# Kernel optimization log

Measured on AMD Instinct MI355X. Metric: run time of the kernel, lower is better.

Reference implementation:

```python
import jax, jax.numpy as jnp
import numpy as np

B, S, D, H = 4, 2048, 256, 8  # batch, seq (context=target), hidden_dim, n_heads


def setup_inputs() -> dict:
    key = jax.random.key(0)
    ks = jax.random.split(key, 12)
    sd = 1.0 / np.sqrt(D)          # torch Linear default init scale (uniform bound)
    sdo = 1.0 / np.sqrt(H * D)
    inp = {
        "k": jax.random.normal(ks[0], (B, S, D), jnp.float32),
        "v": jax.random.normal(ks[1], (B, S, D), jnp.float32),
        "q": jax.random.normal(ks[2], (B, S, D), jnp.float32),
        # Per-head projection weights, stacked over heads. Stored so y = x @ W + b.
        "Wk": jax.random.uniform(ks[3], (H, D, D), jnp.float32, -sd, sd),
        "bk": jax.random.uniform(ks[4], (H, D), jnp.float32, -sd, sd),
        "Wv": jax.random.uniform(ks[5], (H, D, D), jnp.float32, -sd, sd),
        "bv": jax.random.uniform(ks[6], (H, D), jnp.float32, -sd, sd),
        "Wq": jax.random.uniform(ks[7], (H, D, D), jnp.float32, -sd, sd),
        "bq": jax.random.uniform(ks[8], (H, D), jnp.float32, -sd, sd),
        # Final mixing Linear: input is heads interleaved as (hidden, head) flattened,
        # i.e. input index = hid * H + head (torch stack(dim=-1).view order).
        "Wo": jax.random.uniform(ks[9], (H * D, D), jnp.float32, -sdo, sdo),
        "bo": jax.random.uniform(ks[10], (D,), jnp.float32, -sdo, sdo),
    }
    return inp


def reference(k, v, q, Wk, bk, Wv, bv, Wq, bq, Wo, bo):
    # Per-head linear projections (batched over heads instead of a Python loop)
    k_ = jnp.einsum('bmd,hde->bhme', k, Wk) + bk[None, :, None, :]  # [B,H,S,D]
    v_ = jnp.einsum('bmd,hde->bhme', v, Wv) + bv[None, :, None, :]
    q_ = jnp.einsum('bnd,hde->bhne', q, Wq) + bq[None, :, None, :]
    scale = jnp.asarray(np.sqrt(D), k.dtype)
    # dot attention: scores[b,h,n,m] = <q_n, k_m> / sqrt(D); softmax over keys m
    scores = jnp.einsum('bhnd,bhmd->bhnm', q_, k_) / scale
    w = jax.nn.softmax(scores, axis=-1)
    rep = jnp.einsum('bhnm,bhmd->bhnd', w, v_)  # [B,H,S,D]
    # torch: stack(heads, dim=-1) -> [B,S,D,H], then view -> [B,S,D*H] (hid-major)
    outs = rep.transpose(0, 2, 3, 1).reshape(rep.shape[0], rep.shape[2], -1)
    return outs @ Wo + bo
```

## Files before the change

### kernel.cpp

```cpp
#include <hip/hip_runtime.h>

#define BB 4
#define SS 2048
#define DD 256
#define HH 8

typedef unsigned short u16;
typedef __attribute__((ext_vector_type(8))) short bf16x8;
typedef __attribute__((ext_vector_type(4))) float f32x4;
typedef __attribute__((ext_vector_type(16))) float f32x16;
typedef __attribute__((ext_vector_type(4))) short s16x4;

__device__ __forceinline__ f32x4 MFMA(bf16x8 a, bf16x8 b, f32x4 c) {
    return __builtin_amdgcn_mfma_f32_16x16x32_bf16(a, b, c, 0, 0, 0);
}
__device__ __forceinline__ f32x16 MFMA32(bf16x8 a, bf16x8 b, f32x16 c) {
    return __builtin_amdgcn_mfma_f32_32x32x16_bf16(a, b, c, 0, 0, 0);
}

__device__ __forceinline__ u16 f2bf_rtn(float x) {
    unsigned u = __float_as_uint(x);
    u += 0x7FFFu + ((u >> 16) & 1u);
    return (u16)(u >> 16);
}
__device__ __forceinline__ float bf2f(u16 h) {
    return __uint_as_float(((unsigned)h) << 16);
}
__device__ __forceinline__ void split2(float x, u16 &hi, u16 &lo) {
    hi = f2bf_rtn(x);
    lo = f2bf_rtn(x - bf2f(hi));
}

__device__ __forceinline__ void gl_lds16(const u16* g, u16* l) {
    __builtin_amdgcn_global_load_lds(
        (const __attribute__((address_space(1))) unsigned int*)(g),
        (__attribute__((address_space(3))) unsigned int*)(l), 16, 0, 0);
}

__global__ void prep_a3(const float* __restrict__ q, const float* __restrict__ k,
                        const float* __restrict__ v, u16* __restrict__ Q,
                        u16* __restrict__ Kk, u16* __restrict__ V) {
    const size_t i = (size_t)blockIdx.x * 256 + threadIdx.x;
    Q[i]  = f2bf_rtn(q[i]);
    Kk[i] = f2bf_rtn(k[i]);
    V[i]  = f2bf_rtn(v[i]);
}

__global__ void prep_w3(const float* __restrict__ Wq, const float* __restrict__ Wk,
                        const float* __restrict__ Wv,
                        u16* __restrict__ QH2, u16* __restrict__ KH2,
                        u16* __restrict__ VH2, u16* __restrict__ VL2) {
    int n = blockIdx.x;
    int h = n >> 8, e = n & 255;
    int d = threadIdx.x;
    const size_t src = ((size_t)h * 256 + d) * 256 + e;
    const size_t dst = (size_t)n * 256 + d;
    QH2[dst] = f2bf_rtn(Wq[src]);
    KH2[dst] = f2bf_rtn(Wk[src]);
    u16 hi, lo; split2(Wv[src], hi, lo);
    VH2[dst] = hi; VL2[dst] = lo;
}

__global__ void prep_wo(const float* __restrict__ W, u16* __restrict__ Whi,
                        u16* __restrict__ Wlo) {
    int n = blockIdx.x;
    for (int k = threadIdx.x; k < 2048; k += 256) {
        int d = k & 255, h = k >> 8;
        float x = W[((size_t)(d * 8 + h)) * 256 + n];
        u16 hi, lo; split2(x, hi, lo);
        Whi[(size_t)n * 2048 + k] = hi;
        Wlo[(size_t)n * 2048 + k] = lo;
    }
}

__global__ void reduce_out(const float* __restrict__ P, const float* __restrict__ bias,
                           float* __restrict__ out) {
    const int i = blockIdx.x * 1024 + threadIdx.x * 4;
    f32x4 a = *(const f32x4*)(P + i);
    f32x4 b = *(const f32x4*)(P + 2097152 + i);
    f32x4 bv = *(const f32x4*)(bias + ((threadIdx.x * 4) & 255));
    *(f32x4*)(out + i) = (a + b) + bv;
}

template<int MODE, int AMODE, int TERMS, int BN, int LNXB, int SPLK, int BM,
         int DUAL, int NB>
__global__ __launch_bounds__(512, 2) void gemm_split(
    const u16* __restrict__ Ahi, const u16* __restrict__ Alo,
    const u16* __restrict__ Bhi, const u16* __restrict__ Blo,
    const float* __restrict__ bias,
    u16* __restrict__ Ohi,
    float* __restrict__ Of,
    int M, int N, int K, float scale,
    const u16* __restrict__ Ahi2, const u16* __restrict__ Bhi2,
    const float* __restrict__ bias2, u16* __restrict__ Ohi2, float scale2)
{
    constexpr int WN = (BN == 128) ? 4 : 2;
    constexpr int WM = 8 / WN;
    constexpr int MSUB = (BM / WM) / 16;
    constexpr int NSUB = (BN / WN) / 16;
    constexpr int ASZ = BM * 32;
    constexpr int BUFSZ = ASZ * ((TERMS == 3) ? 2 : 1) + 4096 * ((TERMS >= 2) ? 2 : 1);
    constexpr int NBUF = NB;

    __shared__ u16 lds[NBUF * BUFSZ];

    const int tid = threadIdx.x;
    const int lane = tid & 63, wave = tid >> 6;
    const int wm = wave / WN, wn = wave % WN;
    const int nwg = (int)gridDim.x >> (SPLK + DUAL);
    const int half = (SPLK + DUAL) ? ((int)blockIdx.x >= nwg ? 1 : 0) : 0;
    const int b2 = (int)blockIdx.x - half * nwg;
    const int kc = SPLK ? half : 0;
    if (DUAL && half) {
        Ahi = Ahi2; Bhi = Bhi2; bias = bias2; Ohi = Ohi2; scale = scale2;
    }
    const int cpx = nwg >> 3;
    const int wgs = (b2 & 7) * cpx + (b2 >> 3);
    const int m0 = (wgs >> LNXB) * BM;
    const int n0 = (wgs & ((1 << LNXB) - 1)) * BN;
    const int kb = kc * (K >> SPLK);

    f32x4 acc[MSUB][NSUB];
#pragma unroll
    for (int i = 0; i < MSUB; ++i)
#pragma unroll
        for (int j = 0; j < NSUB; ++j) acc[i][j] = {0.f, 0.f, 0.f, 0.f};

    const int rho = tid >> 2;
    const int Xs = (tid & 3) << 3;
    const int ldsW = wave * 512;
    const size_t ga2 = (AMODE == 0) ? (size_t)128 * K : (size_t)128 * DD;

#define G_ISSUE(k0v, p)                                                         \
    {   u16* Bse = lds + (p) * BUFSZ;                                           \
        size_t ga;                                                              \
        if (AMODE == 0)                                                         \
            ga = (size_t)(m0 + rho) * K + (k0v) + Xs;                           \
        else                                                                    \
            ga = ((size_t)((m0 >> 11) * 8 + ((k0v) >> 8)) * SS                  \
                  + (m0 & 2047) + rho) * DD + ((k0v) & 255) + Xs;               \
        gl_lds16(Ahi + ga, Bse + ldsW);                                         \
        if (BM == 256) gl_lds16(Ahi + ga + ga2, Bse + 4096 + ldsW);             \
        if (TERMS == 3) gl_lds16(Alo + ga, Bse + ASZ + 8192 + ldsW);            \
        if (BN == 128 || tid < 256) {                                           \
            size_t gb = (size_t)(n0 + rho) * K + (k0v) + Xs;                    \
            gl_lds16(Bhi + gb, Bse + ASZ + ldsW);                               \
            if (TERMS >= 2) gl_lds16(Blo + gb, Bse + ASZ + 4096 + ldsW);        \
        }                                                                       \
    }

    const int NK = (K >> 5) >> SPLK;
    G_ISSUE(kb, 0);
    if (NBUF == 3) G_ISSUE(kb + 32, 1);

    int buf = 0;
    for (int kt = 0; kt < NK; ++kt) {
        if (NBUF == 3) {
            if (kt < NK - 1) {
                constexpr int W_HI = (BM / 128) * ((TERMS == 3) ? 2 : 1)
                                     + ((TERMS >= 2) ? 2 : 1);
                if (BN == 128) {
                    if constexpr (W_HI == 2)      { asm volatile("s_waitcnt vmcnt(2)" ::: "memory"); }
                    else if constexpr (W_HI == 3) { asm volatile("s_waitcnt vmcnt(3)" ::: "memory"); }
                    else                          { asm volatile("s_waitcnt vmcnt(4)" ::: "memory"); }
                } else {
                    if (wave < 4) { asm volatile("s_waitcnt vmcnt(4)" ::: "memory"); }
                    else          { asm volatile("s_waitcnt vmcnt(2)" ::: "memory"); }
                }
            } else {
                asm volatile("s_waitcnt vmcnt(0)" ::: "memory");
            }
        } else {
            asm volatile("s_waitcnt vmcnt(0)" ::: "memory");
        }
        __builtin_amdgcn_sched_barrier(0);
        __builtin_amdgcn_s_barrier();
        __builtin_amdgcn_sched_barrier(0);

        if (NBUF == 3) {
            if (kt + 2 < NK) {
                const int p2 = (buf + 2 >= 3) ? buf - 1 : buf + 2;
                G_ISSUE(kb + ((kt + 2) << 5), p2);
            }
        } else {
            if (kt + 1 < NK) G_ISSUE(kb + ((kt + 1) << 5), (kt + 1) & 1);
        }

        const u16* Bse = lds + buf * BUFSZ;
        const int g8 = (lane >> 4) << 3;
        const int rA = wm * (BM / WM), rB = wn * (BN / WN);
        bf16x8 bh[NSUB], bl[NSUB];
#pragma unroll
        for (int ns = 0; ns < NSUB; ++ns) {
            const int rb = rB + ns * 16 + (lane & 15);
            bh[ns] = *(const bf16x8*)(Bse + ASZ + rb * 32 + g8);
            if (TERMS >= 2) bl[ns] = *(const bf16x8*)(Bse + ASZ + 4096 + rb * 32 + g8);
        }
#pragma unroll
        for (int ms = 0; ms < MSUB; ++ms) {
            const int ra = rA + ms * 16 + (lane & 15);
            bf16x8 ah = *(const bf16x8*)(Bse + ra * 32 + g8);
            bf16x8 al;
            if (TERMS == 3) al = *(const bf16x8*)(Bse + ASZ + 8192 + ra * 32 + g8);
#pragma unroll
            for (int ns = 0; ns < NSUB; ++ns) {
                acc[ms][ns] = MFMA(ah, bh[ns], acc[ms][ns]);
                if (TERMS == 3) acc[ms][ns] = MFMA(al, bh[ns], acc[ms][ns]);
                if (TERMS >= 2) acc[ms][ns] = MFMA(ah, bl[ns], acc[ms][ns]);
            }
        }
        buf = (buf + 1 == NBUF) ? 0 : buf + 1;
    }
#undef G_ISSUE

#pragma unroll
    for (int ms = 0; ms < MSUB; ++ms)
#pragma unroll
        for (int ns = 0; ns < NSUB; ++ns)
#pragma unroll
            for (int r = 0; r < 4; ++r) {
                int row = m0 + wm * (BM / WM) + ms * 16 + (lane >> 4) * 4 + r;
                int col = n0 + wn * (BN / WN) + ns * 16 + (lane & 15);
                if (MODE == 3) {
                    Of[(size_t)kc * ((size_t)M * N) + (size_t)row * N + col] =
                        acc[ms][ns][r];
                } else {
                    float v = (acc[ms][ns][r] + bias[col]) * scale;
                    if (MODE == 2) {
                        Of[(size_t)row * N + col] = v;
                    } else {
                        int b = row >> 11, s = row & 2047, hh = col >> 8, e = col & 255;
                        size_t idx;
                        if (MODE == 0)
                            idx = ((size_t)(b * HH + hh) * SS + s) * DD + e;
                        else
                            idx = ((size_t)(b * HH + hh) * DD + e) * SS + s;
                        Ohi[idx] = f2bf_rtn(v);
                    }
                }
            }
}

__global__ __launch_bounds__(512, 2) void attn_kernel(
    const u16* __restrict__ Qhi,
    const u16* __restrict__ Khi,
    const u16* __restrict__ Vhi,
    u16* __restrict__ Rhi, u16* __restrict__ Rlo)
{
    __shared__ u16 lK[3][8192];
    __shared__ u16 lV[3][8192];

    const int tid = threadIdx.x, lane = tid & 63, wave = tid >> 6;
    const int qc = lane & 31, g2 = lane >> 5;
    const int wg = ((blockIdx.x & 7) << 5) + (blockIdx.x >> 3);
    const int bh = wg >> 3;
    const int qt = wg & 7;
    const size_t base = (size_t)bh * SS * DD;
    const int q0w = qt * 256 + wave * 32;

    bf16x8 qB[16];
#pragma unroll
    for (int ks = 0; ks < 16; ++ks)
        qB[ks] = *(const bf16x8*)(Qhi + base + (size_t)(q0w + qc) * DD + ks * 16 + g2 * 8);

    int koff[2], voff[2];
#pragma unroll
    for (int i = 0; i < 2; ++i) {
        const int s = tid + i * 512;
        const int kr = s >> 5, kX = s & 31;
        const int kap = (kr & 0x13) | ((kr & 4) << 1) | ((kr & 8) >> 1);
        koff[i] = kap * DD + ((kX ^ kr) << 3);
        const int ve = s >> 2, vXs = s & 3;
        voff[i] = ve * SS + (((vXs ^ ((ve >> 3) & 3))) << 3);
    }

    float l_part = 0.f;
    f32x16 acc[8];
#pragma unroll
    for (int ec = 0; ec < 8; ++ec) acc[ec] = {};

#define ISSUE(tt, p)                                                            \
    {   const u16* Kg = Khi + base + (size_t)(tt) * 32 * DD;                    \
        const u16* Vg = Vhi + base + (size_t)(tt) * 32;                         \
        u16* Kb = &lK[p][0]; u16* Vb = &lV[p][0];                               \
        gl_lds16(Kg + koff[0], Kb + wave * 512);                                \
        gl_lds16(Kg + koff[1], Kb + wave * 512 + 4096);                         \
        gl_lds16(Vg + voff[0], Vb + wave * 512);                                \
        gl_lds16(Vg + voff[1], Vb + wave * 512 + 4096);                         \
    }

    ISSUE(0, 0);
    ISSUE(1, 1);

    for (int t = 0; t < 64; ++t) {
        if (t < 63) { asm volatile("s_waitcnt vmcnt(4)" ::: "memory"); }
        else        { asm volatile("s_waitcnt vmcnt(0)" ::: "memory"); }
        __builtin_amdgcn_sched_barrier(0);
        __builtin_amdgcn_s_barrier();
        __builtin_amdgcn_sched_barrier(0);

        if (t + 2 < 64) ISSUE(t + 2, (t + 2) % 3);

        const u16* Kb = &lK[t % 3][0];
        const u16* Vb = &lV[t % 3][0];

        f32x16 sa = {}, sb = {};
        __builtin_amdgcn_s_setprio(1);
#pragma unroll
        for (int ks = 0; ks < 8; ++ks) {
            bf16x8 ka = *(const bf16x8*)(Kb + qc * DD + (((2 * ks + g2) ^ qc) << 3));
            bf16x8 kb2 = *(const bf16x8*)(Kb + qc * DD + (((2 * (ks + 8) + g2) ^ qc) << 3));
            sa = MFMA32(ka, qB[ks], sa);
            sb = MFMA32(kb2, qB[ks + 8], sb);
        }
        __builtin_amdgcn_s_setprio(0);

        f32x16 s = sa + sb;
#pragma unroll
        for (int n = 0; n < 16; ++n) s[n] = __builtin_amdgcn_exp2f(s[n] - 8.0f);
        float tl = 0.f;
#pragma unroll
        for (int n = 0; n < 16; ++n) tl += s[n];
        l_part += tl;

        bf16x8 p0, p1;
#pragma unroll
        for (int j = 0; j < 4; ++j) {
            unsigned a = __float_as_uint(s[2 * j]);
            unsigned b = __float_as_uint(s[2 * j + 1]);
            ((unsigned*)&p0)[j] = (a >> 16) | (b & 0xffff0000u);
            unsigned c = __float_as_uint(s[8 + 2 * j]);
            unsigned d = __float_as_uint(s[8 + 2 * j + 1]);
            ((unsigned*)&p1)[j] = (c >> 16) | (d & 0xffff0000u);
        }

        __builtin_amdgcn_s_setprio(1);
#pragma unroll
        for (int ec = 0; ec < 8; ++ec) {
            const int e = ec * 32 + qc;
            bf16x8 v0 = *(const bf16x8*)(Vb + e * 32 + (((g2 ^ ((e >> 3) & 3))) << 3));
            bf16x8 v1 = *(const bf16x8*)(Vb + e * 32 + ((((2 + g2) ^ ((e >> 3) & 3))) << 3));
            acc[ec] = MFMA32(v0, p0, acc[ec]);
            acc[ec] = MFMA32(v1, p1, acc[ec]);
        }
        __builtin_amdgcn_s_setprio(0);
    }
#undef ISSUE

    float l = l_part + __shfl_xor(l_part, 32);
    float inv = 1.0f / l;
    const size_t rowbase = ((size_t)bh * SS + q0w + qc) * DD;
#pragma unroll
    for (int ec = 0; ec < 8; ++ec)
#pragma unroll
        for (int rr = 0; rr < 4; ++rr) {
            const int e0 = ec * 32 + 8 * rr + 4 * g2;
            s16x4 hv, lv;
#pragma unroll
            for (int j = 0; j < 4; ++j) {
                u16 h2, l2; split2(acc[ec][4 * rr + j] * inv, h2, l2);
                hv[j] = (short)h2; lv[j] = (short)l2;
            }
            *(s16x4*)(Rhi + rowbase + e0) = hv;
            *(s16x4*)(Rlo + rowbase + e0) = lv;
        }
}

extern "C" void kernel_launch(void* const* d_in, const int* in_sizes, int n_in,
                              void* d_out, int out_size, void* d_ws, size_t ws_size,
                              hipStream_t stream)
{
    (void)in_sizes; (void)n_in; (void)out_size; (void)ws_size;
    const float* k_in = (const float*)d_in[0];
    const float* v_in = (const float*)d_in[1];
    const float* q_in = (const float*)d_in[2];
    const float* Wk   = (const float*)d_in[3];
    const float* bk   = (const float*)d_in[4];
    const float* Wv   = (const float*)d_in[5];
    const float* bv   = (const float*)d_in[6];
    const float* Wq   = (const float*)d_in[7];
    const float* bq   = (const float*)d_in[8];
    const float* Wo   = (const float*)d_in[9];
    const float* bo   = (const float*)d_in[10];
    float* out = (float*)d_out;

    char* p = (char*)d_ws;
    const size_t MB = 1024 * 1024;
    u16* WqH = (u16*)(p + 0 * MB);
    u16* WqL = (u16*)(p + 1 * MB);
    u16* WkH = (u16*)(p + 2 * MB);
    u16* WkL = (u16*)(p + 3 * MB);
    u16* WvH = (u16*)(p + 4 * MB);
    u16* WvL = (u16*)(p + 5 * MB);
    u16* WoH = (u16*)(p + 6 * MB);
    u16* WoL = (u16*)(p + 7 * MB);
    const size_t PB = 32 * MB;
    u16* QH  = (u16*)(p + 8 * MB);
    u16* KH  = (u16*)(p + 8 * MB + 1 * PB);
    u16* VTH = (u16*)(p + 8 * MB + 2 * PB);
    u16* RH  = (u16*)(p + 8 * MB + 3 * PB);
    u16* RL  = (u16*)(p + 8 * MB + 4 * PB);
    u16* AqH = (u16*)(p + 168 * MB);
    u16* AkH = (u16*)(p + 172 * MB);
    u16* AvH = (u16*)(p + 176 * MB);
    float* Pf = (float*)(p + 8 * MB);

    prep_a3<<<dim3(8192), dim3(256), 0, stream>>>(q_in, k_in, v_in, AqH, AkH, AvH);
    prep_w3<<<dim3(2048), dim3(256), 0, stream>>>(Wq, Wk, Wv, WqH, WkH, WvH, WvL);
    prep_wo<<<dim3(256), dim3(256), 0, stream>>>(Wo, WoH, WoL);

    const float qscale = 1.4426950408889634f / 16.0f;
    gemm_split<0, 0, 1, 128, 4, 0, 256, 1, 3><<<dim3(1024), dim3(512), 0, stream>>>(
        AqH, nullptr, WqH, WqL, bq, QH, nullptr, 8192, 2048, 256, qscale,
        AkH, WkH, bk, KH, 1.0f);

    gemm_split<1, 0, 2, 128, 4, 0, 256, 0, 2><<<dim3(512), dim3(512), 0, stream>>>(
        AvH, nullptr, WvH, WvL, bv, VTH, nullptr, 8192, 2048, 256, 1.0f,
        nullptr, nullptr, nullptr, nullptr, 0.f);

    attn_kernel<<<dim3(256), dim3(512), 0, stream>>>(
        QH, KH, VTH, RH, RL);

    gemm_split<3, 2, 3, 64, 2, 1, 128, 0, 2><<<dim3(512), dim3(512), 0, stream>>>(
        RH, RL, WoH, WoL, bo, nullptr, Pf, 8192, 256, 2048, 1.0f,
        nullptr, nullptr, nullptr, nullptr, 0.f);
    reduce_out<<<dim3(2048), dim3(256), 0, stream>>>(Pf, bo, out);
}
```

Before: 273.9 us.

## Double-buffer 64-key tiles instead of triple-buffering 32-key tiles in attention

The attention loop now streams 64-key K/V tiles into two LDS buffers, replacing the triple-buffered 32-key tiles, which halves the number of barriers and wait points per head. The swizzle patterns for K and V are rebuilt for the wider tiles, and each iteration runs two 32-key sub-steps. The cost is that the prefetch depth drops to a single tile with a full vmcnt(0) wait each iteration, so load latency may be exposed. LDS use also grows, from 96KB to 128KB per block, which may limit occupancy under launch_bounds(512,2).

```diff
diff --git a/kernel.cpp b/kernel.cpp
--- a/kernel.cpp
+++ b/kernel.cpp
@@ -247,8 +247,8 @@
     const u16* __restrict__ Vhi,
     u16* __restrict__ Rhi, u16* __restrict__ Rlo)
 {
-    __shared__ u16 lK[3][8192];
-    __shared__ u16 lV[3][8192];
+    __shared__ u16 lK[2][16384];
+    __shared__ u16 lV[2][16384];
 
     const int tid = threadIdx.x, lane = tid & 63, wave = tid >> 6;
     const int qc = lane & 31, g2 = lane >> 5;
@@ -263,15 +263,15 @@
     for (int ks = 0; ks < 16; ++ks)
         qB[ks] = *(const bf16x8*)(Qhi + base + (size_t)(q0w + qc) * DD + ks * 16 + g2 * 8);
 
-    int koff[2], voff[2];
-#pragma unroll
-    for (int i = 0; i < 2; ++i) {
+    int koff[4], voff[4];
+#pragma unroll
+    for (int i = 0; i < 4; ++i) {
         const int s = tid + i * 512;
         const int kr = s >> 5, kX = s & 31;
-        const int kap = (kr & 0x13) | ((kr & 4) << 1) | ((kr & 8) >> 1);
-        koff[i] = kap * DD + ((kX ^ kr) << 3);
-        const int ve = s >> 2, vXs = s & 3;
-        voff[i] = ve * SS + (((vXs ^ ((ve >> 3) & 3))) << 3);
+        const int kap = (kr & 0x33) | ((kr & 4) << 1) | ((kr & 8) >> 1);
+        koff[i] = kap * DD + ((kX ^ (kr & 31)) << 3);
+        const int ve = s >> 3, vXs = s & 7;
+        voff[i] = ve * SS + ((vXs ^ (ve & 7)) << 3);
     }
 
     float l_part = 0.f;
@@ -280,70 +280,76 @@
     for (int ec = 0; ec < 8; ++ec) acc[ec] = {};
 
 #define ISSUE(tt, p)                                                            \
-    {   const u16* Kg = Khi + base + (size_t)(tt) * 32 * DD;                    \
-        const u16* Vg = Vhi + base + (size_t)(tt) * 32;                         \
-        u16* Kb = &lK[p][0]; u16* Vb = &lV[p][0];                               \
-        gl_lds16(Kg + koff[0], Kb + wave * 512);                                \
-        gl_lds16(Kg + koff[1], Kb + wave * 512 + 4096);                         \
-        gl_lds16(Vg + voff[0], Vb + wave * 512);                                \
-        gl_lds16(Vg + voff[1], Vb + wave * 512 + 4096);                         \
+    {   const u16* Kg = Khi + base + (size_t)(tt) * 64 * DD;                    \
+        const u16* Vg = Vhi + base + (size_t)(tt) * 64;                         \
+        u16* Kb_ = &lK[p][0]; u16* Vb_ = &lV[p][0];                             \
+        _Pragma("unroll")                                                       \
+        for (int i = 0; i < 4; ++i) {                                           \
+            gl_lds16(Kg + koff[i], Kb_ + wave * 512 + i * 4096);                \
+            gl_lds16(Vg + voff[i], Vb_ + wave * 512 + i * 4096);                \
+        }                                                                       \
     }
 
     ISSUE(0, 0);
-    ISSUE(1, 1);
-
-    for (int t = 0; t < 64; ++t) {
-        if (t < 63) { asm volatile("s_waitcnt vmcnt(4)" ::: "memory"); }
-        else        { asm volatile("s_waitcnt vmcnt(0)" ::: "memory"); }
+
+    for (int t = 0; t < 32; ++t) {
+        asm volatile("s_waitcnt vmcnt(0)" ::: "memory");
         __builtin_amdgcn_sched_barrier(0);
         __builtin_amdgcn_s_barrier();
         __builtin_amdgcn_sched_barrier(0);
 
-        if (t + 2 < 64) ISSUE(t + 2, (t + 2) % 3);
-
-        const u16* Kb = &lK[t % 3][0];
-        const u16* Vb = &lV[t % 3][0];
-
-        f32x16 sa = {}, sb = {};
-        __builtin_amdgcn_s_setprio(1);
-#pragma unroll
-        for (int ks = 0; ks < 8; ++ks) {
-            bf16x8 ka = *(const bf16x8*)(Kb + qc * DD + (((2 * ks + g2) ^ qc) << 3));
-            bf16x8 kb2 = *(const bf16x8*)(Kb + qc * DD + (((2 * (ks + 8) + g2) ^ qc) << 3));
-            sa = MFMA32(ka, qB[ks], sa);
-            sb = MFMA32(kb2, qB[ks + 8], sb);
-        }
-        __builtin_amdgcn_s_setprio(0);
-
-        f32x16 s = sa + sb;
-#pragma unroll
-        for (int n = 0; n < 16; ++n) s[n] = __builtin_amdgcn_exp2f(s[n] - 8.0f);
-        float tl = 0.f;
-#pragma unroll
-        for (int n = 0; n < 16; ++n) tl += s[n];
-        l_part += tl;
-
-        bf16x8 p0, p1;
-#pragma unroll
-        for (int j = 0; j < 4; ++j) {
-            unsigned a = __float_as_uint(s[2 * j]);
-            unsigned b = __float_as_uint(s[2 * j + 1]);
-            ((unsigned*)&p0)[j] = (a >> 16) | (b & 0xffff0000u);
-            unsigned c = __float_as_uint(s[8 + 2 * j]);
-            unsigned d = __float_as_uint(s[8 + 2 * j + 1]);
-            ((unsigned*)&p1)[j] = (c >> 16) | (d & 0xffff0000u);
-        }
-
-        __builtin_amdgcn_s_setprio(1);
-#pragma unroll
-        for (int ec = 0; ec < 8; ++ec) {
-            const int e = ec * 32 + qc;
-            bf16x8 v0 = *(const bf16x8*)(Vb + e * 32 + (((g2 ^ ((e >> 3) & 3))) << 3));
-            bf16x8 v1 = *(const bf16x8*)(Vb + e * 32 + ((((2 + g2) ^ ((e >> 3) & 3))) << 3));
-            acc[ec] = MFMA32(v0, p0, acc[ec]);
-            acc[ec] = MFMA32(v1, p1, acc[ec]);
-        }
-        __builtin_amdgcn_s_setprio(0);
+        if (t + 1 < 32) ISSUE(t + 1, (t + 1) & 1);
+
+        const u16* Kb = &lK[t & 1][0];
+        const u16* Vb = &lV[t & 1][0];
+
+#pragma unroll
+        for (int ks2 = 0; ks2 < 2; ++ks2) {
+            f32x16 sa = {}, sb = {};
+            __builtin_amdgcn_s_setprio(1);
+#pragma unroll
+            for (int ks = 0; ks < 8; ++ks) {
+                bf16x8 ka = *(const bf16x8*)(Kb + (ks2 * 32 + qc) * DD +
+                                             (((2 * ks + g2) ^ qc) << 3));
+                bf16x8 kb2 = *(const bf16x8*)(Kb + (ks2 * 32 + qc) * DD +
+                                              (((2 * (ks + 8) + g2) ^ qc) << 3));
+                sa = MFMA32(ka, qB[ks], sa);
+                sb = MFMA32(kb2, qB[ks + 8], sb);
+            }
+            __builtin_amdgcn_s_setprio(0);
+
+            f32x16 s = sa + sb;
+#pragma unroll
+            for (int n = 0; n < 16; ++n) s[n] = __builtin_amdgcn_exp2f(s[n] - 8.0f);
+            float tl = 0.f;
+#pragma unroll
+            for (int n = 0; n < 16; ++n) tl += s[n];
+            l_part += tl;
+
+            bf16x8 p0, p1;
+#pragma unroll
+            for (int j = 0; j < 4; ++j) {
+                unsigned a = __float_as_uint(s[2 * j]);
+                unsigned b = __float_as_uint(s[2 * j + 1]);
+                ((unsigned*)&p0)[j] = (a >> 16) | (b & 0xffff0000u);
+                unsigned c = __float_as_uint(s[8 + 2 * j]);
+                unsigned d = __float_as_uint(s[8 + 2 * j + 1]);
+                ((unsigned*)&p1)[j] = (c >> 16) | (d & 0xffff0000u);
+            }
+
+            __builtin_amdgcn_s_setprio(1);
+#pragma unroll
+            for (int ec = 0; ec < 8; ++ec) {
+                const int e = ec * 32 + qc;
+                bf16x8 v0 = *(const bf16x8*)(Vb + e * 64 +
+                                             (((4 * ks2 + g2) ^ (e & 7)) << 3));
+                bf16x8 v1 = *(const bf16x8*)(Vb + e * 64 +
+                                             (((4 * ks2 + 2 + g2) ^ (e & 7)) << 3));
+                acc[ec] = MFMA32(v0, p0, acc[ec]);
+                acc[ec] = MFMA32(v1, p1, acc[ec]);
+            }
+            __builtin_amdgcn_s_setprio(0);
+        }
     }
 #undef ISSUE
 
```

After: 347.5 us. 1.27x slower.
